# Performance work log

Measured on AMD Instinct MI355X. Metric: run time of the kernel, lower is better.

## Reference

```python
import jax, jax.numpy as jnp
import numpy as np

BSZ, P, D, C = 16, 4096, 256, 512


def setup_inputs() -> dict:
    key = jax.random.key(0)
    k1, k2 = jax.random.split(key)
    x = jax.random.normal(k1, (BSZ, P, D), dtype=jnp.float32)
    kernels = jax.random.normal(k2, (C, D), dtype=jnp.float32) * 0.001
    return {"x": x, "kernels": kernels}


def reference(x, kernels):
    bsz, Pn, d = x.shape
    # (bsz, P, C) projection scores, ReLU'd
    scores = jax.nn.relu(jnp.einsum('bpd,cd->bpc', x, kernels))
    # per-channel argmax over positions -> (bsz, C)
    idx = jnp.argmax(scores, axis=1)
    # scatter_add each kernel row into its winning position
    b_idx = jnp.arange(bsz)[:, None]  # (bsz, 1) broadcast against (bsz, C)
    src = jnp.broadcast_to(kernels, (bsz,) + kernels.shape)  # (bsz, C, d)
    out = jnp.zeros((bsz, Pn, d), dtype=x.dtype).at[b_idx, idx].add(src)
    return out
```

## Files before the change

kernel.cpp:

```cpp
#include <hip/hip_runtime.h>
#include <cstddef>
#include <cstdint>

#define BSZ 16
#define PN  4096
#define DD  256
#define CC  512
#define TP  128
#define TC  128
#define NPT (PN / TP)
#define NKC 8

typedef short bf16x8 __attribute__((ext_vector_type(8)));
typedef float f32x4  __attribute__((ext_vector_type(4)));

struct Top2 { float v1, v2; int i1, i2; };

__device__ __forceinline__ void t2_insert(Top2& t, float v, int i) {
  if (v > t.v1 || (v == t.v1 && i < t.i1)) {
    t.v2 = t.v1; t.i2 = t.i1; t.v1 = v; t.i1 = i;
  } else if (v > t.v2 || (v == t.v2 && i < t.i2)) {
    t.v2 = v; t.i2 = i;
  }
}

__device__ __forceinline__ void split4(float4 v, uint2& hp, uint2& lp) {
  uint32_t u0 = __float_as_uint(v.x), u1 = __float_as_uint(v.y),
           u2 = __float_as_uint(v.z), u3 = __float_as_uint(v.w);
  float l0 = v.x - __uint_as_float(u0 & 0xffff0000u);
  float l1 = v.y - __uint_as_float(u1 & 0xffff0000u);
  float l2 = v.z - __uint_as_float(u2 & 0xffff0000u);
  float l3 = v.w - __uint_as_float(u3 & 0xffff0000u);
  hp.x = __builtin_amdgcn_perm(u1, u0, 0x07060302u);
  hp.y = __builtin_amdgcn_perm(u3, u2, 0x07060302u);
  lp.x = __builtin_amdgcn_perm(__float_as_uint(l1), __float_as_uint(l0), 0x07060302u);
  lp.y = __builtin_amdgcn_perm(__float_as_uint(l3), __float_as_uint(l2), 0x07060302u);
}

__device__ __forceinline__ void gld16(const void* gsrc, void* ldst) {
  __builtin_amdgcn_global_load_lds(
      (const __attribute__((address_space(1))) unsigned int*)gsrc,
      (__attribute__((address_space(3))) unsigned int*)ldst, 16, 0, 0);
}

__global__ __launch_bounds__(256) void convert_x_kernel(
    const float* __restrict__ x, uint32_t* __restrict__ xs) {
  const int kc = blockIdx.x, pt = blockIdx.y, b = blockIdx.z;
  const size_t chunk = (((size_t)b * NPT + pt) * NKC + kc) * 4096;
#pragma unroll
  for (int s0 = 0; s0 < 2; s0++) {
    int s  = threadIdx.x + s0 * 256;
    int fp = s >> 6, kg = (s >> 4) & 3, lr = s & 15;
    int r  = fp * 16 + lr, k0 = kg * 8;
    const float* src = x + ((size_t)b * PN + (size_t)pt * TP + r) * DD + kc * 32 + k0;
    float4 v0 = *(const float4*)src, v1 = *(const float4*)(src + 4);
    uint2 h0, l0, h1, l1; split4(v0, h0, l0); split4(v1, h1, l1);
    *(uint4*)&xs[chunk + (size_t)s * 4]        = make_uint4(h0.x, h0.y, h1.x, h1.y);
    *(uint4*)&xs[chunk + 2048 + (size_t)s * 4] = make_uint4(l0.x, l0.y, l1.x, l1.y);
  }
}

__global__ __launch_bounds__(256) void convert_k_kernel(
    const float* __restrict__ kern, uint32_t* __restrict__ ks) {
  const int kc = blockIdx.x, ct = blockIdx.y;
  const size_t chunk = ((size_t)ct * NKC + kc) * 4096;
#pragma unroll
  for (int s0 = 0; s0 < 2; s0++) {
    int s  = threadIdx.x + s0 * 256;
    int fp = s >> 6, kg = (s >> 4) & 3, lr = s & 15;
    int r  = fp * 16 + lr, k0 = kg * 8;
    const float* src = kern + ((size_t)ct * TC + r) * DD + kc * 32 + k0;
    float4 v0 = *(const float4*)src, v1 = *(const float4*)(src + 4);
    uint2 h0, l0, h1, l1; split4(v0, h0, l0); split4(v1, h1, l1);
    *(uint4*)&ks[chunk + (size_t)s * 4]        = make_uint4(h0.x, h0.y, h1.x, h1.y);
    *(uint4*)&ks[chunk + 2048 + (size_t)s * 4] = make_uint4(l0.x, l0.y, l1.x, l1.y);
  }
}

__global__ __launch_bounds__(256) void score_kernel(
    const uint32_t* __restrict__ xs, const uint32_t* __restrict__ ks,
    float2* __restrict__ pv2, uint32_t* __restrict__ pix) {

  __shared__ __align__(16) short lds[2 * 8192];
  short* As = lds;
  short* Bs = lds + 8192;

  const int ct = blockIdx.x, pt = blockIdx.y, b = blockIdx.z;
  const int tid  = threadIdx.x;
  const int lane = tid & 63, wave = tid >> 6;
  const int wr = wave >> 1, wc = wave & 1;
  const int lr = lane & 15, kg = lane >> 4;

  const char* xsb = (const char*)xs + (((size_t)b * NPT + pt) * NKC) * 16384;
  const char* ksb = (const char*)ks + ((size_t)ct * NKC) * 16384;

  f32x4 acc[4][4];
#pragma unroll
  for (int i = 0; i < 4; i++)
#pragma unroll
    for (int j = 0; j < 4; j++) acc[i][j] = (f32x4)0.f;

  for (int kc = 0; kc < NKC; kc++) {
    const char* asrc = xsb + kc * 16384 + tid * 16;
    const char* bsrc = ksb + kc * 16384 + tid * 16;
    char* adst = (char*)As + tid * 16;
    char* bdst = (char*)Bs + tid * 16;
#pragma unroll
    for (int i = 0; i < 4; i++) {
      gld16(asrc + i * 4096, adst + i * 4096);
      gld16(bsrc + i * 4096, bdst + i * 4096);
    }
    __syncthreads();

    bf16x8 Ah[4], Al[4];
    const int aoff = wr * 2048 + lane * 8;
#pragma unroll
    for (int fp = 0; fp < 4; fp++) {
      Ah[fp] = *(const bf16x8*)&As[aoff + fp * 512];
      Al[fp] = *(const bf16x8*)&As[4096 + aoff + fp * 512];
    }
    const int boff = wc * 2048 + lane * 8;
#pragma unroll
    for (int fc = 0; fc < 4; fc++) {
      bf16x8 Bh = *(const bf16x8*)&Bs[boff + fc * 512];
      bf16x8 Bl = *(const bf16x8*)&Bs[4096 + boff + fc * 512];
#pragma unroll
      for (int fp = 0; fp < 4; fp++) {
        acc[fp][fc] = __builtin_amdgcn_mfma_f32_16x16x32_bf16(Ah[fp], Bh, acc[fp][fc], 0, 0, 0);
        acc[fp][fc] = __builtin_amdgcn_mfma_f32_16x16x32_bf16(Ah[fp], Bl, acc[fp][fc], 0, 0, 0);
        acc[fp][fc] = __builtin_amdgcn_mfma_f32_16x16x32_bf16(Al[fp], Bh, acc[fp][fc], 0, 0, 0);
      }
    }
    __syncthreads();
  }

  float4* scratch = (float4*)lds;
  const int slot = wr * 4 + kg;
#pragma unroll
  for (int fc = 0; fc < 4; fc++) {
    Top2 t; t.v1 = -1.f; t.v2 = -1.f; t.i1 = 0x7fffffff; t.i2 = 0x7fffffff;
#pragma unroll
    for (int fp = 0; fp < 4; fp++)
#pragma unroll
      for (int r = 0; r < 4; r++) {
        float v = acc[fp][fc][r]; v = v > 0.f ? v : 0.f;
        t2_insert(t, v, wr * 64 + fp * 16 + kg * 4 + r);
      }
    int c_local = wc * 64 + fc * 16 + lr;
    scratch[slot * TC + c_local] =
        make_float4(t.v1, __int_as_float(t.i1), t.v2, __int_as_float(t.i2));
  }
  __syncthreads();

  if (tid < TC) {
    Top2 t; t.v1 = -1.f; t.v2 = -1.f; t.i1 = 0x7fffffff; t.i2 = 0x7fffffff;
#pragma unroll
    for (int s = 0; s < 8; s++) {
      float4 e = scratch[s * TC + tid];
      t2_insert(t, e.x, __float_as_int(e.y));
      t2_insert(t, e.z, __float_as_int(e.w));
    }
    int c = ct * TC + tid;
    size_t o = ((size_t)b * CC + c) * NPT + pt;
    uint32_t p1 = (uint32_t)(pt * TP + t.i1);
    uint32_t p2 = (uint32_t)(pt * TP + t.i2);
    pv2[o] = make_float2(t.v1, t.v2);
    pix[o] = (p1 << 16) | (p2 & 0xffffu);
  }
}

__global__ __launch_bounds__(64) void reduce_winner_kernel(
    const float2* __restrict__ pv2, const uint32_t* __restrict__ pix,
    const float* __restrict__ x, const float* __restrict__ kern,
    int* __restrict__ winner) {
  const int c = blockIdx.x, b = blockIdx.y;
  const int l = threadIdx.x;

  Top2 t; t.v1 = -1.f; t.v2 = -1.f; t.i1 = 0x7fffffff; t.i2 = 0x7fffffff;
  if (l < NPT) {
    size_t o = ((size_t)b * CC + c) * NPT + l;
    float2 v = pv2[o]; uint32_t ii = pix[o];
    t.v1 = v.x; t.v2 = v.y; t.i1 = (int)(ii >> 16); t.i2 = (int)(ii & 0xffffu);
  }
#pragma unroll
  for (int m = 1; m < 64; m <<= 1) {
    float uv1 = __shfl_xor(t.v1, m, 64);
    int   ui1 = __shfl_xor(t.i1, m, 64);
    float uv2 = __shfl_xor(t.v2, m, 64);
    int   ui2 = __shfl_xor(t.i2, m, 64);
    t2_insert(t, uv1, ui1);
    t2_insert(t, uv2, ui2);
  }

  int win = t.i1;
  if (t.v1 - t.v2 <= 1e-4f * t.v1 + 1e-5f) {
    const float4* x1 = (const float4*)(x + ((size_t)b * PN + t.i1) * DD);
    const float4* x2 = (const float4*)(x + ((size_t)b * PN + t.i2) * DD);
    const float4* kc = (const float4*)(kern + (size_t)c * DD);
    float4 a1 = x1[l], a2 = x2[l], k4 = kc[l];
    float s1 = a1.x * k4.x + a1.y * k4.y + a1.z * k4.z + a1.w * k4.w;
    float s2 = a2.x * k4.x + a2.y * k4.y + a2.z * k4.z + a2.w * k4.w;
#pragma unroll
    for (int m = 1; m < 64; m <<= 1) {
      s1 += __shfl_xor(s1, m, 64);
      s2 += __shfl_xor(s2, m, 64);
    }
    s1 = fmaxf(s1, 0.f); s2 = fmaxf(s2, 0.f);
    if (s2 > s1 || (s2 == s1 && t.i2 < t.i1)) win = t.i2;
  }
  if (l == 0) winner[(size_t)b * CC + c] = win;
}

__global__ __launch_bounds__(64) void write_out_kernel(
    const int* __restrict__ winner, const float* __restrict__ kern,
    float4* __restrict__ out) {
  const int p = blockIdx.x, b = blockIdx.y;
  const int l = threadIdx.x;
  const int* wb = winner + (size_t)b * CC;

  int4 w0 = *(const int4*)&wb[l * 8];
  int4 w1 = *(const int4*)&wb[l * 8 + 4];
  int wv[8] = {w0.x, w0.y, w0.z, w0.w, w1.x, w1.y, w1.z, w1.w};

  float4 acc = make_float4(0.f, 0.f, 0.f, 0.f);
#pragma unroll
  for (int j = 0; j < 8; j++) {
    unsigned long long m = __ballot(wv[j] == p);
    while (m) {
      int bit = __ffsll((long long)m) - 1; m &= m - 1;
      int c = bit * 8 + j;
      float4 kv = ((const float4*)(kern + (size_t)c * DD))[l];
      acc.x += kv.x; acc.y += kv.y; acc.z += kv.z; acc.w += kv.w;
    }
  }
  out[((size_t)b * PN + p) * 64 + l] = acc;
}

extern "C" void kernel_launch(void* const* d_in, const int* in_sizes, int n_in,
                              void* d_out, int out_size, void* d_ws, size_t ws_size,
                              hipStream_t stream) {
  const float* x    = (const float*)d_in[0];
  const float* kern = (const float*)d_in[1];
  float* out = (float*)d_out;

  uint32_t* xs = (uint32_t*)d_out;

  char* ws = (char*)d_ws;
  float2*   pv2 = (float2*)ws;
  uint32_t* pix = (uint32_t*)(ws + (size_t)BSZ * CC * NPT * sizeof(float2));
  uint32_t* ks  = (uint32_t*)(ws + 3u * 1024 * 1024);
  int*      win = (int*)(ws + 3u * 1024 * 1024 + 512u * 1024);

  convert_k_kernel<<<dim3(NKC, CC / TC), 256, 0, stream>>>(kern, ks);
  convert_x_kernel<<<dim3(NKC, NPT, BSZ), 256, 0, stream>>>(x, xs);

  score_kernel<<<dim3(CC / TC, NPT, BSZ), 256, 0, stream>>>(xs, ks, pv2, pix);

  reduce_winner_kernel<<<dim3(CC, BSZ), 64, 0, stream>>>(pv2, pix, x, kern, win);

  write_out_kernel<<<dim3(PN, BSZ), 64, 0, stream>>>(win, kern, (float4*)out);
}
```

Before: 220.3 us.

## Fuse x bf16 split into score kernel with double-buffered LDS loads

Removes the separate convert_x pass. The score kernel now loads raw fp32 x tiles directly into LDS and splits them into hi/lo bf16 in registers, which drops a full write and re-read of the converted x buffer. The main loop is double-buffered with explicit vmcnt waits and barriers, so the next K-chunk's global-to-LDS loads overlap with the MFMA work. The write-out kernel now handles four positions per 256-thread block and stages the winner row in LDS. The cost is 64KB of LDS per block, which lowers occupancy, plus extra conversion ALU work inside the GEMM loop, which is repeated across the four channel tiles.

```diff
diff --git a/kernel.cpp b/kernel.cpp
--- a/kernel.cpp
+++ b/kernel.cpp
@@ -13,6 +13,10 @@
 
 typedef short bf16x8 __attribute__((ext_vector_type(8)));
 typedef float f32x4  __attribute__((ext_vector_type(4)));
+
+#define MEMFENCE() __asm__ __volatile__("" ::: "memory")
+#define WAITCNT_VM8 0x1F78
+#define WAITCNT_VM0 0x1F70
 
 struct Top2 { float v1, v2; int i1, i2; };
 
@@ -43,23 +47,6 @@
       (__attribute__((address_space(3))) unsigned int*)ldst, 16, 0, 0);
 }
 
-__global__ __launch_bounds__(256) void convert_x_kernel(
-    const float* __restrict__ x, uint32_t* __restrict__ xs) {
-  const int kc = blockIdx.x, pt = blockIdx.y, b = blockIdx.z;
-  const size_t chunk = (((size_t)b * NPT + pt) * NKC + kc) * 4096;
-#pragma unroll
-  for (int s0 = 0; s0 < 2; s0++) {
-    int s  = threadIdx.x + s0 * 256;
-    int fp = s >> 6, kg = (s >> 4) & 3, lr = s & 15;
-    int r  = fp * 16 + lr, k0 = kg * 8;
-    const float* src = x + ((size_t)b * PN + (size_t)pt * TP + r) * DD + kc * 32 + k0;
-    float4 v0 = *(const float4*)src, v1 = *(const float4*)(src + 4);
-    uint2 h0, l0, h1, l1; split4(v0, h0, l0); split4(v1, h1, l1);
-    *(uint4*)&xs[chunk + (size_t)s * 4]        = make_uint4(h0.x, h0.y, h1.x, h1.y);
-    *(uint4*)&xs[chunk + 2048 + (size_t)s * 4] = make_uint4(l0.x, l0.y, l1.x, l1.y);
-  }
-}
-
 __global__ __launch_bounds__(256) void convert_k_kernel(
     const float* __restrict__ kern, uint32_t* __restrict__ ks) {
   const int kc = blockIdx.x, ct = blockIdx.y;
@@ -78,21 +65,26 @@
 }
 
 __global__ __launch_bounds__(256) void score_kernel(
-    const uint32_t* __restrict__ xs, const uint32_t* __restrict__ ks,
+    const float* __restrict__ x, const uint32_t* __restrict__ ks,
     float2* __restrict__ pv2, uint32_t* __restrict__ pix) {
 
-  __shared__ __align__(16) short lds[2 * 8192];
-  short* As = lds;
-  short* Bs = lds + 8192;
+  __shared__ __align__(16) char lds[65536];
 
   const int ct = blockIdx.x, pt = blockIdx.y, b = blockIdx.z;
   const int tid  = threadIdx.x;
   const int lane = tid & 63, wave = tid >> 6;
   const int wr = wave >> 1, wc = wave & 1;
-  const int lr = lane & 15, kg = lane >> 4;
-
-  const char* xsb = (const char*)xs + (((size_t)b * NPT + pt) * NKC) * 16384;
-  const char* ksb = (const char*)ks + ((size_t)ct * NKC) * 16384;
+
+  const char* xbase = (const char*)(x + ((size_t)b * PN + (size_t)pt * TP) * DD);
+  const char* asrc[4];
+#pragma unroll
+  for (int i = 0; i < 4; i++) {
+    int s = i * 256 + tid;
+    int swr = s >> 9, sfp = (s >> 7) & 3, sl = (s >> 1) & 63, sh = s & 1;
+    int row = swr * 64 + sfp * 16 + (sl & 15);
+    asrc[i] = xbase + (size_t)row * (DD * 4) + (sl >> 4) * 32 + sh * 16;
+  }
+  const char* bsrc = (const char*)ks + ((size_t)ct * NKC) * 16384 + tid * 16;
 
   f32x4 acc[4][4];
 #pragma unroll
@@ -100,30 +92,48 @@
 #pragma unroll
     for (int j = 0; j < 4; j++) acc[i][j] = (f32x4)0.f;
 
+  auto issue = [&](int kc) {
+    char* Ab = lds + (kc & 1) * 16384;
+    char* Bb = lds + 32768 + (kc & 1) * 16384;
+#pragma unroll
+    for (int i = 0; i < 4; i++)
+      gld16(asrc[i] + kc * 128, Ab + i * 4096 + tid * 16);
+#pragma unroll
+    for (int i = 0; i < 4; i++)
+      gld16(bsrc + kc * 16384 + i * 4096, Bb + i * 4096 + tid * 16);
+  };
+
+  issue(0);
   for (int kc = 0; kc < NKC; kc++) {
-    const char* asrc = xsb + kc * 16384 + tid * 16;
-    const char* bsrc = ksb + kc * 16384 + tid * 16;
-    char* adst = (char*)As + tid * 16;
-    char* bdst = (char*)Bs + tid * 16;
-#pragma unroll
-    for (int i = 0; i < 4; i++) {
-      gld16(asrc + i * 4096, adst + i * 4096);
-      gld16(bsrc + i * 4096, bdst + i * 4096);
-    }
-    __syncthreads();
+    if (kc + 1 < NKC) issue(kc + 1);
+    MEMFENCE();
+    if (kc + 1 < NKC) {
+      __builtin_amdgcn_s_waitcnt(WAITCNT_VM8);
+    } else {
+      __builtin_amdgcn_s_waitcnt(WAITCNT_VM0);
+    }
+    __builtin_amdgcn_s_barrier();
+    MEMFENCE();
+
+    const char* Ab = lds + (kc & 1) * 16384;
+    const char* Bb = lds + 32768 + (kc & 1) * 16384;
 
     bf16x8 Ah[4], Al[4];
-    const int aoff = wr * 2048 + lane * 8;
 #pragma unroll
     for (int fp = 0; fp < 4; fp++) {
-      Ah[fp] = *(const bf16x8*)&As[aoff + fp * 512];
-      Al[fp] = *(const bf16x8*)&As[4096 + aoff + fp * 512];
-    }
-    const int boff = wc * 2048 + lane * 8;
+      const float4* ap = (const float4*)(Ab + wr * 8192 + fp * 2048 + lane * 32);
+      float4 v0 = ap[0], v1 = ap[1];
+      uint2 h0, l0, h1, l1; split4(v0, h0, l0); split4(v1, h1, l1);
+      uint4 hh = make_uint4(h0.x, h0.y, h1.x, h1.y);
+      uint4 ll = make_uint4(l0.x, l0.y, l1.x, l1.y);
+      Ah[fp] = *(bf16x8*)&hh;
+      Al[fp] = *(bf16x8*)&ll;
+    }
 #pragma unroll
     for (int fc = 0; fc < 4; fc++) {
-      bf16x8 Bh = *(const bf16x8*)&Bs[boff + fc * 512];
-      bf16x8 Bl = *(const bf16x8*)&Bs[4096 + boff + fc * 512];
+      const char* bp = Bb + wc * 4096 + fc * 1024 + lane * 16;
+      bf16x8 Bh = *(const bf16x8*)bp;
+      bf16x8 Bl = *(const bf16x8*)(bp + 8192);
 #pragma unroll
       for (int fp = 0; fp < 4; fp++) {
         acc[fp][fc] = __builtin_amdgcn_mfma_f32_16x16x32_bf16(Ah[fp], Bh, acc[fp][fc], 0, 0, 0);
@@ -131,9 +141,13 @@
         acc[fp][fc] = __builtin_amdgcn_mfma_f32_16x16x32_bf16(Al[fp], Bh, acc[fp][fc], 0, 0, 0);
       }
     }
-    __syncthreads();
-  }
-
+    MEMFENCE();
+    __builtin_amdgcn_s_barrier();
+    MEMFENCE();
+  }
+  __syncthreads();
+
+  const int lr = lane & 15, kg = lane >> 4;
   float4* scratch = (float4*)lds;
   const int slot = wr * 4 + kg;
 #pragma unroll
@@ -211,15 +225,19 @@
   if (l == 0) winner[(size_t)b * CC + c] = win;
 }
 
-__global__ __launch_bounds__(64) void write_out_kernel(
+__global__ __launch_bounds__(256) void write_out_kernel(
     const int* __restrict__ winner, const float* __restrict__ kern,
     float4* __restrict__ out) {
-  const int p = blockIdx.x, b = blockIdx.y;
-  const int l = threadIdx.x;
-  const int* wb = winner + (size_t)b * CC;
-
-  int4 w0 = *(const int4*)&wb[l * 8];
-  int4 w1 = *(const int4*)&wb[l * 8 + 4];
+  __shared__ __align__(16) int wrow[CC];
+  const int b = blockIdx.y;
+  const int tid = threadIdx.x, lane = tid & 63, w = tid >> 6;
+  const int p = blockIdx.x * 4 + w;
+
+  *(int2*)&wrow[tid * 2] = *(const int2*)&winner[(size_t)b * CC + tid * 2];
+  __syncthreads();
+
+  int4 w0 = *(const int4*)&wrow[lane * 8];
+  int4 w1 = *(const int4*)&wrow[lane * 8 + 4];
   int wv[8] = {w0.x, w0.y, w0.z, w0.w, w1.x, w1.y, w1.z, w1.w};
 
   float4 acc = make_float4(0.f, 0.f, 0.f, 0.f);
@@ -229,11 +247,11 @@
     while (m) {
       int bit = __ffsll((long long)m) - 1; m &= m - 1;
       int c = bit * 8 + j;
-      float4 kv = ((const float4*)(kern + (size_t)c * DD))[l];
+      float4 kv = ((const float4*)(kern + (size_t)c * DD))[lane];
       acc.x += kv.x; acc.y += kv.y; acc.z += kv.z; acc.w += kv.w;
     }
   }
-  out[((size_t)b * PN + p) * 64 + l] = acc;
+  out[((size_t)b * PN + p) * 64 + lane] = acc;
 }
 
 extern "C" void kernel_launch(void* const* d_in, const int* in_sizes, int n_in,
@@ -243,8 +261,6 @@
   const float* kern = (const float*)d_in[1];
   float* out = (float*)d_out;
 
-  uint32_t* xs = (uint32_t*)d_out;
-
   char* ws = (char*)d_ws;
   float2*   pv2 = (float2*)ws;
   uint32_t* pix = (uint32_t*)(ws + (size_t)BSZ * CC * NPT * sizeof(float2));
@@ -252,11 +268,10 @@
   int*      win = (int*)(ws + 3u * 1024 * 1024 + 512u * 1024);
 
   convert_k_kernel<<<dim3(NKC, CC / TC), 256, 0, stream>>>(kern, ks);
-  convert_x_kernel<<<dim3(NKC, NPT, BSZ), 256, 0, stream>>>(x, xs);
-
-  score_kernel<<<dim3(CC / TC, NPT, BSZ), 256, 0, stream>>>(xs, ks, pv2, pix);
+
+  score_kernel<<<dim3(CC / TC, NPT, BSZ), 256, 0, stream>>>(x, ks, pv2, pix);
 
   reduce_winner_kernel<<<dim3(CC, BSZ), 64, 0, stream>>>(pv2, pix, x, kern, win);
 
-  write_out_kernel<<<dim3(PN, BSZ), 64, 0, stream>>>(win, kern, (float4*)out);
-}
+  write_out_kernel<<<dim3(PN / 4, BSZ), 256, 0, stream>>>(win, kern, (float4*)out);
+}
```

Result: faster. 199.4 us (-9.5%).
